# Kernel optimization log

Hardware: AMD Instinct MI355X
Metric: run time of the kernel (lower is better)

## Reference

```python
import jax, jax.numpy as jnp
import numpy as np

DIM = 256
HEADS = 4
DIM_HEAD = 32
HIDDEN = HEADS * DIM_HEAD  # 128
EPS = 1e-5


def setup_inputs() -> dict:
    key = jax.random.key(0)
    ks = jax.random.split(key, 6)
    B, H, W = 16, 64, 64
    x = jax.random.normal(ks[0], (B, DIM, H, W), dtype=jnp.float32)
    # 1x1 conv weights stored as [out_ch, in_ch]
    W_qkv = jax.random.normal(ks[1], (HIDDEN * 3, DIM), dtype=jnp.float32) * 0.02
    W_out = jax.random.normal(ks[2], (DIM, HIDDEN), dtype=jnp.float32) * 0.02
    b_out = jnp.zeros((DIM,), dtype=jnp.float32)
    gamma = jnp.ones((DIM,), dtype=jnp.float32)
    beta = jnp.zeros((DIM,), dtype=jnp.float32)
    return {"x": x, "W_qkv": W_qkv, "W_out": W_out, "b_out": b_out,
            "gamma": gamma, "beta": beta}


def reference(x, W_qkv, W_out, b_out, gamma, beta):
    b, c, h, w = x.shape
    n = h * w
    scale = DIM_HEAD ** -0.5
    # 1x1 conv == channel matmul
    qkv = jnp.einsum('bchw,oc->bohw', x, W_qkv)  # [b, 3*hidden, h, w]
    q, k, v = jnp.split(qkv, 3, axis=1)
    def to_heads(t):
        return t.reshape(b, HEADS, DIM_HEAD, n)  # b h d n
    q = jax.nn.softmax(to_heads(q), axis=-2) * scale  # softmax over d
    k = jax.nn.softmax(to_heads(k), axis=-1)           # softmax over n
    v = to_heads(v)
    # context: [b, h, d, e] — tiny 32x32 per head
    context = jnp.einsum('bhdn,bhen->bhde', k, v)
    out = jnp.einsum('bhde,bhdn->bhen', context, q)  # [b, h, e, n]
    out = out.reshape(b, HIDDEN, h, w)
    # output 1x1 conv with bias
    out = jnp.einsum('bchw,oc->bohw', out, W_out) + b_out[None, :, None, None]
    # GroupNorm(1, dim): normalize over (C,H,W) per sample, per-channel affine
    mean = out.mean(axis=(1, 2, 3), keepdims=True)
    var = out.var(axis=(1, 2, 3), keepdims=True)
    out = (out - mean) * jax.lax.rsqrt(var + EPS)
    return out * gamma[None, :, None, None] + beta[None, :, None, None]
```

## Files before the change

kernel.cpp:

```cpp
#include <hip/hip_runtime.h>

#define NN 4096
#define CIN 256
#define O3 384
#define HID 128
#define NHEAD 4
#define DH 32

typedef float f32x4 __attribute__((ext_vector_type(4)));
typedef _Float16 f16x8 __attribute__((ext_vector_type(8)));
typedef _Float16 f16x4 __attribute__((ext_vector_type(4)));
typedef _Float16 f16x2 __attribute__((ext_vector_type(2)));
typedef __fp16 fp16x2_raw __attribute__((ext_vector_type(2)));

__device__ __forceinline__ f16x2 pkrtz(float a, float b) {
  fp16x2_raw r = __builtin_amdgcn_cvt_pkrtz(a, b);
  return __builtin_bit_cast(f16x2, r);
}

__global__ __launch_bounds__(256) void prep(
    const float* __restrict__ Wqkv, const float* __restrict__ Wout,
    _Float16* __restrict__ WpkA, _Float16* __restrict__ WpkB,
    float* __restrict__ zbase, int nz) {
  const int bid = blockIdx.x, tid = threadIdx.x;
  if (bid < 48) {
    int t = bid * 256 + tid;
    int l = t & 63, mk = t >> 6;
    int k32 = mk & 7, m16 = mk >> 3;
    int row = m16 * 16 + (l & 15), k = k32 * 32 + (l >> 4) * 8;
    const float* s = Wqkv + (size_t)row * CIN + k;
    f16x8 o;
#pragma unroll
    for (int j = 0; j < 8; j++) o[j] = (_Float16)s[j];
    *(f16x8*)(WpkA + (size_t)t * 8) = o;
  } else if (bid < 64) {
    int t = (bid - 48) * 256 + tid;
    int l = t & 63, mk = t >> 6;
    int k32 = mk & 3, m16 = mk >> 2;
    int row = m16 * 16 + (l & 15), k = k32 * 32 + (l >> 4) * 8;
    const float* s = Wout + (size_t)row * HID + k;
    f16x8 o;
#pragma unroll
    for (int j = 0; j < 8; j++) o[j] = (_Float16)s[j];
    *(f16x8*)(WpkB + (size_t)t * 8) = o;
  } else {
    int i = (bid - 64) * 256 + tid;
    if (i < nz) zbase[i] = 0.f;
  }
}

__global__ __launch_bounds__(256) void gemm_qkv(
    const float* __restrict__ X, const _Float16* __restrict__ Wpk,
    _Float16* __restrict__ Yt) {
  __shared__ _Float16 Bs[128][40];
  const int mt = blockIdx.x;
  const int n0 = blockIdx.y * 128;
  const int b = blockIdx.z;
  const float* Xb = X + (size_t)b * CIN * NN;
  _Float16* Yb = Yt + (size_t)b * NN * O3;
  const int tid = threadIdx.x, l = tid & 63, wid = tid >> 6;
  const int wm = (wid >> 1) << 6, wn = (wid & 1) << 6;
  const int fr = l & 15, q = l >> 4, kq = q << 3;
  const int b_n = (tid & 31) << 2, b_kk = (tid >> 5) << 2;
  const int am16 = mt * 8 + (wm >> 4);

  f32x4 acc[4][4];
#pragma unroll
  for (int i = 0; i < 4; i++)
#pragma unroll
    for (int j = 0; j < 4; j++) acc[i][j] = (f32x4){0.f, 0.f, 0.f, 0.f};

  for (int k0 = 0; k0 < CIN; k0 += 32) {
    float xr[4][4];
#pragma unroll
    for (int i = 0; i < 4; i++)
      *(float4*)xr[i] = *(const float4*)(Xb + (size_t)(k0 + b_kk + i) * NN + n0 + b_n);
    f16x8 ah[4];
#pragma unroll
    for (int fm = 0; fm < 4; fm++)
      ah[fm] = *(const f16x8*)(Wpk + ((size_t)((am16 + fm) * 8 + (k0 >> 5)) * 64 + l) * 8);
    __syncthreads();
#pragma unroll
    for (int j = 0; j < 4; j++) {
      f16x2 p0 = pkrtz(xr[0][j], xr[1][j]);
      f16x2 p1 = pkrtz(xr[2][j], xr[3][j]);
      *(f16x4*)&Bs[b_n + j][b_kk] = (f16x4){p0[0], p0[1], p1[0], p1[1]};
    }
    __syncthreads();
    f16x8 bh[4];
#pragma unroll
    for (int fn = 0; fn < 4; fn++)
      bh[fn] = *(const f16x8*)&Bs[wn + fn * 16 + fr][kq];
#pragma unroll
    for (int fm = 0; fm < 4; fm++)
#pragma unroll
      for (int fn = 0; fn < 4; fn++)
        acc[fm][fn] = __builtin_amdgcn_mfma_f32_16x16x32_f16(ah[fm], bh[fn], acc[fm][fn], 0, 0, 0);
  }
#pragma unroll
  for (int fm = 0; fm < 4; fm++) {
    int mrow = mt * 128 + wm + fm * 16 + q * 4;
#pragma unroll
    for (int fn = 0; fn < 4; fn++) {
      int n = n0 + wn + fn * 16 + fr;
      f16x2 h0 = pkrtz(acc[fm][fn][0], acc[fm][fn][1]);
      f16x2 h1 = pkrtz(acc[fm][fn][2], acc[fm][fn][3]);
      *(f16x4*)(Yb + (size_t)n * O3 + mrow) = (f16x4){h0[0], h0[1], h1[0], h1[1]};
    }
  }
}

__global__ __launch_bounds__(256) void attn1(
    const _Float16* __restrict__ qkvt, float* __restrict__ ctx_raw,
    float* __restrict__ srow_raw) {
  const int h = blockIdx.x, b = blockIdx.y, ns = blockIdx.z;
  const _Float16* base = qkvt + (size_t)b * NN * O3;
  const _Float16* Kb = base + HID + h * DH;
  const _Float16* Vb = base + 2 * HID + h * DH;
  float* ctx = ctx_raw + (size_t)(b * NHEAD + h) * (DH * DH);
  float* srow = srow_raw + (size_t)(b * NHEAD + h) * DH;
  __shared__ __align__(16) float Es[64][36];
  __shared__ __align__(16) float Vs[64][36];
  __shared__ float ctxs[DH][DH + 1];
  __shared__ float srow_s[DH];
  const int tid = threadIdx.x, l = tid & 63, w = tid >> 6;
  const int d4 = (l >> 3) << 2, e4 = (l & 7) << 2;
  if (tid < DH) srow_s[tid] = 0.f;
  for (int i = tid; i < DH * (DH + 1); i += 256) (&ctxs[0][0])[i] = 0.f;
  float sacc[4] = {0.f, 0.f, 0.f, 0.f};
  float acc[4][4];
#pragma unroll
  for (int i = 0; i < 4; i++)
#pragma unroll
    for (int j = 0; j < 4; j++) acc[i][j] = 0.f;

  for (int c = 0; c < 8; c++) {
    const int n0 = ns * 512 + c * 64;
    const size_t roff = (size_t)(n0 + l) * O3 + w * 8;
    f16x8 kv = *(const f16x8*)(Kb + roff);
    f16x8 vv = *(const f16x8*)(Vb + roff);
    __syncthreads();
    float4 e0, e1, v0, v1;
    e0.x = __expf((float)kv[0]); e0.y = __expf((float)kv[1]);
    e0.z = __expf((float)kv[2]); e0.w = __expf((float)kv[3]);
    e1.x = __expf((float)kv[4]); e1.y = __expf((float)kv[5]);
    e1.z = __expf((float)kv[6]); e1.w = __expf((float)kv[7]);
    v0.x = (float)vv[0]; v0.y = (float)vv[1]; v0.z = (float)vv[2]; v0.w = (float)vv[3];
    v1.x = (float)vv[4]; v1.y = (float)vv[5]; v1.z = (float)vv[6]; v1.w = (float)vv[7];
    *(float4*)&Es[l][w * 8] = e0;
    *(float4*)&Es[l][w * 8 + 4] = e1;
    *(float4*)&Vs[l][w * 8] = v0;
    *(float4*)&Vs[l][w * 8 + 4] = v1;
    __syncthreads();
#pragma unroll
    for (int it = 0; it < 16; it++) {
      const int n = w + 4 * it;
      float ka[4], va[4];
      *(float4*)ka = *(const float4*)&Es[n][d4];
      *(float4*)va = *(const float4*)&Vs[n][e4];
#pragma unroll
      for (int i = 0; i < 4; i++) {
        sacc[i] += ka[i];
#pragma unroll
        for (int j = 0; j < 4; j++) acc[i][j] = fmaf(ka[i], va[j], acc[i][j]);
      }
    }
  }
  if ((l & 7) == 0) {
#pragma unroll
    for (int i = 0; i < 4; i++) atomicAdd(&srow_s[d4 + i], sacc[i]);
  }
#pragma unroll
  for (int i = 0; i < 4; i++)
#pragma unroll
    for (int j = 0; j < 4; j++) atomicAdd(&ctxs[d4 + i][e4 + j], acc[i][j]);
  __syncthreads();
  for (int i = tid; i < DH * DH; i += 256) atomicAdd(&ctx[i], ctxs[i >> 5][i & 31]);
  if (tid < DH) atomicAdd(&srow[tid], srow_s[tid]);
}

__global__ __launch_bounds__(256) void attn2(
    _Float16* __restrict__ qkvt, const float* __restrict__ ctx_raw,
    const float* __restrict__ srow_raw) {
  const int ns = blockIdx.x, h = blockIdx.y, b = blockIdx.z;
  const float* cg = ctx_raw + (size_t)(b * NHEAD + h) * (DH * DH);
  const float* sr = srow_raw + (size_t)(b * NHEAD + h) * DH;
  __shared__ float ctxs[DH][DH + 1];
  const int tid = threadIdx.x;
  for (int i = tid; i < DH * DH; i += 256) ctxs[i >> 5][i & 31] = cg[i] / sr[i >> 5];
  __syncthreads();
  const int n = ns * 256 + tid;
  _Float16* qp = qkvt + ((size_t)b * NN + n) * O3 + h * DH;
  float qv[DH];
#pragma unroll
  for (int i = 0; i < 4; i++) {
    f16x8 v = *(const f16x8*)(qp + i * 8);
#pragma unroll
    for (int j = 0; j < 8; j++) qv[i * 8 + j] = (float)v[j];
  }
  float m = -1e30f;
#pragma unroll
  for (int d = 0; d < DH; d++) m = fmaxf(m, qv[d]);
  float s = 0.f;
#pragma unroll
  for (int d = 0; d < DH; d++) { qv[d] = __expf(qv[d] - m); s += qv[d]; }
  float inv = 0.17677669529663687f / s;
#pragma unroll
  for (int d = 0; d < DH; d++) qv[d] *= inv;
#pragma unroll
  for (int eo = 0; eo < 4; eo++) {
    float o[8];
#pragma unroll
    for (int j = 0; j < 8; j++) o[j] = 0.f;
#pragma unroll
    for (int d = 0; d < DH; d++) {
      float qd = qv[d];
#pragma unroll
      for (int j = 0; j < 8; j++) o[j] = fmaf(ctxs[d][eo * 8 + j], qd, o[j]);
    }
    f16x2 h0 = pkrtz(o[0], o[1]);
    f16x2 h1 = pkrtz(o[2], o[3]);
    f16x2 h2 = pkrtz(o[4], o[5]);
    f16x2 h3 = pkrtz(o[6], o[7]);
    f16x8 ov = (f16x8){h0[0], h0[1], h1[0], h1[1], h2[0], h2[1], h3[0], h3[1]};
    *(f16x8*)(qp + eo * 8) = ov;
  }
}

__global__ __launch_bounds__(256) void gemm_proj(
    const _Float16* __restrict__ At, const _Float16* __restrict__ Wpk,
    const float* __restrict__ bias, float* __restrict__ out,
    double* __restrict__ stats) {
  __shared__ _Float16 Bs[128][40];
  const int mt = blockIdx.x;
  const int n0 = blockIdx.y * 128;
  const int b = blockIdx.z;
  const _Float16* Ab = At + (size_t)b * NN * O3;
  float* outb = out + (size_t)b * CIN * NN;
  const int tid = threadIdx.x, l = tid & 63, wid = tid >> 6;
  const int wm = (wid >> 1) << 6, wn = (wid & 1) << 6;
  const int fr = l & 15, q = l >> 4, kq = q << 3;
  const int am16 = mt * 8 + (wm >> 4);
  const int sr0 = tid >> 2, sc = (tid & 3) << 3;

  f32x4 acc[4][4];
#pragma unroll
  for (int i = 0; i < 4; i++)
#pragma unroll
    for (int j = 0; j < 4; j++) acc[i][j] = (f32x4){0.f, 0.f, 0.f, 0.f};

  for (int k0 = 0; k0 < HID; k0 += 32) {
    f16x8 v0 = *(const f16x8*)(Ab + (size_t)(n0 + sr0) * O3 + k0 + sc);
    f16x8 v1 = *(const f16x8*)(Ab + (size_t)(n0 + 64 + sr0) * O3 + k0 + sc);
    f16x8 ah[4];
#pragma unroll
    for (int fm = 0; fm < 4; fm++)
      ah[fm] = *(const f16x8*)(Wpk + ((size_t)((am16 + fm) * 4 + (k0 >> 5)) * 64 + l) * 8);
    __syncthreads();
    *(f16x8*)&Bs[sr0][sc] = v0;
    *(f16x8*)&Bs[64 + sr0][sc] = v1;
    __syncthreads();
    f16x8 bh[4];
#pragma unroll
    for (int fn = 0; fn < 4; fn++)
      bh[fn] = *(const f16x8*)&Bs[wn + fn * 16 + fr][kq];
#pragma unroll
    for (int fm = 0; fm < 4; fm++)
#pragma unroll
      for (int fn = 0; fn < 4; fn++)
        acc[fm][fn] = __builtin_amdgcn_mfma_f32_16x16x32_f16(ah[fm], bh[fn], acc[fm][fn], 0, 0, 0);
  }
  float lsum = 0.f, lsq = 0.f;
#pragma unroll
  for (int fm = 0; fm < 4; fm++) {
    int rowb = mt * 128 + wm + fm * 16 + q * 4;
#pragma unroll
    for (int r = 0; r < 4; r++) {
      float bv = bias[rowb + r];
      float* dst = outb + (size_t)(rowb + r) * NN + n0 + wn + fr;
#pragma unroll
      for (int fn = 0; fn < 4; fn++) {
        float v = acc[fm][fn][r] + bv;
        dst[fn * 16] = v;
        lsum += v;
        lsq += v * v;
      }
    }
  }
  double ds = (double)lsum, dq = (double)lsq;
#pragma unroll
  for (int off = 32; off; off >>= 1) {
    ds += __shfl_down(ds, off);
    dq += __shfl_down(dq, off);
  }
  __shared__ double sred[8];
  if (l == 0) { sred[wid] = ds; sred[4 + wid] = dq; }
  __syncthreads();
  if (tid == 0) {
    atomicAdd(&stats[b * 2 + 0], sred[0] + sred[1] + sred[2] + sred[3]);
    atomicAdd(&stats[b * 2 + 1], sred[4] + sred[5] + sred[6] + sred[7]);
  }
}

__global__ __launch_bounds__(256) void gn_norm(
    float* __restrict__ out, const double* __restrict__ stats,
    const float* __restrict__ gamma, const float* __restrict__ beta) {
  const int b = blockIdx.y;
  const double nels = (double)CIN * (double)NN;
  double S = stats[b * 2 + 0], Q2 = stats[b * 2 + 1];
  double mu = S / nels;
  double var = Q2 / nels - mu * mu;
  float mean = (float)mu;
  float rstd = (float)rsqrt(var + 1e-5);
  size_t i4 = (size_t)blockIdx.x * 256 + threadIdx.x;
  int c = (int)((i4 * 4) >> 12);
  float g = gamma[c] * rstd, bt = beta[c];
  float4* p = (float4*)(out + (size_t)b * CIN * NN) + i4;
  float4 v = *p;
  v.x = (v.x - mean) * g + bt;
  v.y = (v.y - mean) * g + bt;
  v.z = (v.z - mean) * g + bt;
  v.w = (v.w - mean) * g + bt;
  *p = v;
}

extern "C" void kernel_launch(void* const* d_in, const int* in_sizes, int n_in,
                              void* d_out, int out_size, void* d_ws, size_t ws_size,
                              hipStream_t stream) {
  const float* x     = (const float*)d_in[0];
  const float* Wqkv  = (const float*)d_in[1];
  const float* Wout  = (const float*)d_in[2];
  const float* bout  = (const float*)d_in[3];
  const float* gamma = (const float*)d_in[4];
  const float* beta  = (const float*)d_in[5];
  float* out = (float*)d_out;

  char* ws = (char*)d_ws;
  _Float16* qkvt = (_Float16*)ws;
  size_t off = (size_t)16 * NN * O3 * 2;
  _Float16* WpkA = (_Float16*)(ws + off); off += 48 * 256 * 8 * 2;
  _Float16* WpkB = (_Float16*)(ws + off); off += 16 * 256 * 8 * 2;
  float* ctxg = (float*)(ws + off); off += (size_t)16 * NHEAD * DH * DH * 4;
  float* srow = (float*)(ws + off); off += (size_t)16 * NHEAD * DH * 4;
  double* stats = (double*)(ws + off);

  const int nz = 16 * NHEAD * DH * DH + 16 * NHEAD * DH + 64;
  prep<<<64 + (nz + 255) / 256, 256, 0, stream>>>(Wqkv, Wout, WpkA, WpkB, ctxg, nz);
  gemm_qkv<<<dim3(3, 32, 16), 256, 0, stream>>>(x, WpkA, qkvt);
  attn1<<<dim3(NHEAD, 16, 8), 256, 0, stream>>>(qkvt, ctxg, srow);
  attn2<<<dim3(16, NHEAD, 16), 256, 0, stream>>>(qkvt, ctxg, srow);
  gemm_proj<<<dim3(2, 32, 16), 256, 0, stream>>>(qkvt, WpkB, bout, out, stats);
  gn_norm<<<dim3(1024, 16), 256, 0, stream>>>(out, stats, gamma, beta);
}
```

Measured before the change: 141.8 us.

## Stage full-K X tile in LDS once and loop over all QKV output tiles

The QKV projection kernel now loads a 64-column slab of X across all 256 input channels into shared memory once, converting it to fp16. Each block then loops over all three 128-row output tiles, so X is read from global memory once instead of three times. The per-k-step double sync is removed, at the cost of a larger shared-memory footprint, fewer columns per block and a smaller per-warp MFMA tile. It also raises the occupancy hint in launch bounds.

```diff
diff --git a/kernel.cpp b/kernel.cpp
--- a/kernel.cpp
+++ b/kernel.cpp
@@ -49,63 +49,77 @@
   }
 }
 
-__global__ __launch_bounds__(256) void gemm_qkv(
+__global__ __launch_bounds__(256, 4) void gemm_qkv(
     const float* __restrict__ X, const _Float16* __restrict__ Wpk,
     _Float16* __restrict__ Yt) {
-  __shared__ _Float16 Bs[128][40];
-  const int mt = blockIdx.x;
-  const int n0 = blockIdx.y * 128;
-  const int b = blockIdx.z;
+  __shared__ _Float16 Xs[8][64][40];
+  const int tid = threadIdx.x;
+  const int n0 = blockIdx.x * 64;
+  const int b = blockIdx.y;
   const float* Xb = X + (size_t)b * CIN * NN;
   _Float16* Yb = Yt + (size_t)b * NN * O3;
-  const int tid = threadIdx.x, l = tid & 63, wid = tid >> 6;
-  const int wm = (wid >> 1) << 6, wn = (wid & 1) << 6;
+
+  const int sc = tid & 15;
+  const int skq = (tid >> 4) * 4;
+  f32x4 xv[4][4];
+#pragma unroll
+  for (int ch = 0; ch < 4; ch++) {
+    const int kbase = ch * 64 + skq;
+#pragma unroll
+    for (int r = 0; r < 4; r++)
+      xv[ch][r] = *(const f32x4*)(Xb + (size_t)(kbase + r) * NN + n0 + sc * 4);
+  }
+#pragma unroll
+  for (int ch = 0; ch < 4; ch++) {
+    const int kb = ch * 2 + (skq >> 5);
+    const int kk = skq & 31;
+#pragma unroll
+    for (int j = 0; j < 4; j++) {
+      f16x2 p0 = pkrtz(xv[ch][0][j], xv[ch][1][j]);
+      f16x2 p1 = pkrtz(xv[ch][2][j], xv[ch][3][j]);
+      *(f16x4*)&Xs[kb][sc * 4 + j][kk] = (f16x4){p0[0], p0[1], p1[0], p1[1]};
+    }
+  }
+  __syncthreads();
+
+  const int l = tid & 63, w = tid >> 6;
+  const int wrow = (w >> 1) << 6;
+  const int wcol = (w & 1) << 5;
   const int fr = l & 15, q = l >> 4, kq = q << 3;
-  const int b_n = (tid & 31) << 2, b_kk = (tid >> 5) << 2;
-  const int am16 = mt * 8 + (wm >> 4);
-
-  f32x4 acc[4][4];
-#pragma unroll
-  for (int i = 0; i < 4; i++)
-#pragma unroll
-    for (int j = 0; j < 4; j++) acc[i][j] = (f32x4){0.f, 0.f, 0.f, 0.f};
-
-  for (int k0 = 0; k0 < CIN; k0 += 32) {
-    float xr[4][4];
+
+  for (int mtl = 0; mtl < 3; ++mtl) {
+    f32x4 acc[4][2];
 #pragma unroll
     for (int i = 0; i < 4; i++)
-      *(float4*)xr[i] = *(const float4*)(Xb + (size_t)(k0 + b_kk + i) * NN + n0 + b_n);
-    f16x8 ah[4];
-#pragma unroll
-    for (int fm = 0; fm < 4; fm++)
-      ah[fm] = *(const f16x8*)(Wpk + ((size_t)((am16 + fm) * 8 + (k0 >> 5)) * 64 + l) * 8);
-    __syncthreads();
-#pragma unroll
-    for (int j = 0; j < 4; j++) {
-      f16x2 p0 = pkrtz(xr[0][j], xr[1][j]);
-      f16x2 p1 = pkrtz(xr[2][j], xr[3][j]);
-      *(f16x4*)&Bs[b_n + j][b_kk] = (f16x4){p0[0], p0[1], p1[0], p1[1]};
-    }
-    __syncthreads();
-    f16x8 bh[4];
-#pragma unroll
-    for (int fn = 0; fn < 4; fn++)
-      bh[fn] = *(const f16x8*)&Bs[wn + fn * 16 + fr][kq];
-#pragma unroll
-    for (int fm = 0; fm < 4; fm++)
-#pragma unroll
-      for (int fn = 0; fn < 4; fn++)
-        acc[fm][fn] = __builtin_amdgcn_mfma_f32_16x16x32_f16(ah[fm], bh[fn], acc[fm][fn], 0, 0, 0);
-  }
-#pragma unroll
-  for (int fm = 0; fm < 4; fm++) {
-    int mrow = mt * 128 + wm + fm * 16 + q * 4;
-#pragma unroll
-    for (int fn = 0; fn < 4; fn++) {
-      int n = n0 + wn + fn * 16 + fr;
-      f16x2 h0 = pkrtz(acc[fm][fn][0], acc[fm][fn][1]);
-      f16x2 h1 = pkrtz(acc[fm][fn][2], acc[fm][fn][3]);
-      *(f16x4*)(Yb + (size_t)n * O3 + mrow) = (f16x4){h0[0], h0[1], h1[0], h1[1]};
+#pragma unroll
+      for (int j = 0; j < 2; j++) acc[i][j] = (f32x4){0.f, 0.f, 0.f, 0.f};
+    const int am16 = mtl * 8 + (wrow >> 4);
+#pragma unroll
+    for (int kb = 0; kb < 8; ++kb) {
+      f16x8 ah[4];
+#pragma unroll
+      for (int fm = 0; fm < 4; fm++)
+        ah[fm] = *(const f16x8*)(Wpk + ((size_t)((am16 + fm) * 8 + kb) * 64 + l) * 8);
+      f16x8 bh[2];
+#pragma unroll
+      for (int fn = 0; fn < 2; fn++)
+        bh[fn] = *(const f16x8*)&Xs[kb][wcol + fn * 16 + fr][kq];
+#pragma unroll
+      for (int fm = 0; fm < 4; fm++)
+#pragma unroll
+        for (int fn = 0; fn < 2; fn++)
+          acc[fm][fn] = __builtin_amdgcn_mfma_f32_16x16x32_f16(ah[fm], bh[fn], acc[fm][fn], 0, 0, 0);
+    }
+#pragma unroll
+    for (int fm = 0; fm < 4; fm++) {
+      int mrow = mtl * 128 + wrow + fm * 16 + q * 4;
+#pragma unroll
+      for (int fn = 0; fn < 2; fn++) {
+        int n = n0 + wcol + fn * 16 + fr;
+        f16x2 h0 = pkrtz(acc[fm][fn][0], acc[fm][fn][1]);
+        f16x2 h1 = pkrtz(acc[fm][fn][2], acc[fm][fn][3]);
+        *(f16x4*)(Yb + (size_t)n * O3 + mrow) = (f16x4){h0[0], h0[1], h1[0], h1[1]};
+      }
     }
   }
 }
@@ -346,7 +360,7 @@
 
   const int nz = 16 * NHEAD * DH * DH + 16 * NHEAD * DH + 64;
   prep<<<64 + (nz + 255) / 256, 256, 0, stream>>>(Wqkv, Wout, WpkA, WpkB, ctxg, nz);
-  gemm_qkv<<<dim3(3, 32, 16), 256, 0, stream>>>(x, WpkA, qkvt);
+  gemm_qkv<<<dim3(64, 16), 256, 0, stream>>>(x, WpkA, qkvt);
   attn1<<<dim3(NHEAD, 16, 8), 256, 0, stream>>>(qkvt, ctxg, srow);
   attn2<<<dim3(16, NHEAD, 16), 256, 0, stream>>>(qkvt, ctxg, srow);
   gemm_proj<<<dim3(2, 32, 16), 256, 0, stream>>>(qkvt, WpkB, bout, out, stats);
```

Result: slower. 167.5 us (+18.1%).

## Double-buffer QKV GEMM shared tiles with register prefetch and XCD-aware block swizzle

Applied to the files above, without the earlier changes.

The QKV projection GEMM now keeps two LDS buffers and prefetches the next X tile and weight fragments into registers while the MFMAs for the current tile run. This cuts the K-loop from two barriers per step to one. The grid is flattened to 1D, and block indices are remapped so consecutive blocks on the same XCD share the same X columns across the three M tiles, which should improve L2 reuse. The cost is more registers and LDS per block, which may lower occupancy.

```diff
diff --git a/kernel.cpp b/kernel.cpp
--- a/kernel.cpp
+++ b/kernel.cpp
@@ -52,10 +52,13 @@
 __global__ __launch_bounds__(256) void gemm_qkv(
     const float* __restrict__ X, const _Float16* __restrict__ Wpk,
     _Float16* __restrict__ Yt) {
-  __shared__ _Float16 Bs[128][40];
-  const int mt = blockIdx.x;
-  const int n0 = blockIdx.y * 128;
-  const int b = blockIdx.z;
+  __shared__ _Float16 Bs[2][128][40];
+  const int orig = blockIdx.x;
+  const int swz = (orig & 7) * 192 + (orig >> 3);
+  const int mt = swz % 3;
+  const int nb = swz / 3;
+  const int n0 = (nb & 31) << 7;
+  const int b  = nb >> 5;
   const float* Xb = X + (size_t)b * CIN * NN;
   _Float16* Yb = Yt + (size_t)b * NN * O3;
   const int tid = threadIdx.x, l = tid & 63, wid = tid >> 6;
@@ -64,39 +67,62 @@
   const int b_n = (tid & 31) << 2, b_kk = (tid >> 5) << 2;
   const int am16 = mt * 8 + (wm >> 4);
 
+#define LOADX(dst, t_) do { \
+    _Pragma("unroll") \
+    for (int r_ = 0; r_ < 4; r_++) \
+      dst[r_] = *(const f32x4*)(Xb + (size_t)((t_) * 32 + b_kk + r_) * NN + n0 + b_n); \
+  } while (0)
+#define LOADAH(dst, t_) do { \
+    _Pragma("unroll") \
+    for (int fm_ = 0; fm_ < 4; fm_++) \
+      dst[fm_] = *(const f16x8*)(Wpk + ((size_t)((am16 + fm_) * 8 + (t_)) * 64 + l) * 8); \
+  } while (0)
+#define CVTW(buf_, src) do { \
+    _Pragma("unroll") \
+    for (int j_ = 0; j_ < 4; j_++) { \
+      f16x2 p0_ = pkrtz(src[0][j_], src[1][j_]); \
+      f16x2 p1_ = pkrtz(src[2][j_], src[3][j_]); \
+      *(f16x4*)&Bs[buf_][b_n + j_][b_kk] = (f16x4){p0_[0], p0_[1], p1_[0], p1_[1]}; \
+    } } while (0)
+
+  f32x4 xr[2][4];
+  f16x8 ah[2][4];
   f32x4 acc[4][4];
 #pragma unroll
   for (int i = 0; i < 4; i++)
 #pragma unroll
     for (int j = 0; j < 4; j++) acc[i][j] = (f32x4){0.f, 0.f, 0.f, 0.f};
 
-  for (int k0 = 0; k0 < CIN; k0 += 32) {
-    float xr[4][4];
-#pragma unroll
-    for (int i = 0; i < 4; i++)
-      *(float4*)xr[i] = *(const float4*)(Xb + (size_t)(k0 + b_kk + i) * NN + n0 + b_n);
-    f16x8 ah[4];
+  LOADX(xr[0], 0);
+  CVTW(0, xr[0]);
+  LOADAH(ah[0], 0);
+  LOADX(xr[1], 1);
+  asm volatile("s_waitcnt lgkmcnt(0)" ::: "memory");
+  __builtin_amdgcn_s_barrier();
+  __builtin_amdgcn_sched_barrier(0);
+
+#pragma unroll
+  for (int t = 0; t < 8; t++) {
+    const int cur = t & 1, nxt = cur ^ 1;
+    f16x8 bh[4];
+#pragma unroll
+    for (int fn = 0; fn < 4; fn++)
+      bh[fn] = *(const f16x8*)&Bs[cur][wn + fn * 16 + fr][kq];
 #pragma unroll
     for (int fm = 0; fm < 4; fm++)
-      ah[fm] = *(const f16x8*)(Wpk + ((size_t)((am16 + fm) * 8 + (k0 >> 5)) * 64 + l) * 8);
-    __syncthreads();
-#pragma unroll
-    for (int j = 0; j < 4; j++) {
-      f16x2 p0 = pkrtz(xr[0][j], xr[1][j]);
-      f16x2 p1 = pkrtz(xr[2][j], xr[3][j]);
-      *(f16x4*)&Bs[b_n + j][b_kk] = (f16x4){p0[0], p0[1], p1[0], p1[1]};
-    }
-    __syncthreads();
-    f16x8 bh[4];
-#pragma unroll
-    for (int fn = 0; fn < 4; fn++)
-      bh[fn] = *(const f16x8*)&Bs[wn + fn * 16 + fr][kq];
-#pragma unroll
-    for (int fm = 0; fm < 4; fm++)
 #pragma unroll
       for (int fn = 0; fn < 4; fn++)
-        acc[fm][fn] = __builtin_amdgcn_mfma_f32_16x16x32_f16(ah[fm], bh[fn], acc[fm][fn], 0, 0, 0);
-  }
+        acc[fm][fn] = __builtin_amdgcn_mfma_f32_16x16x32_f16(ah[cur][fm], bh[fn], acc[fm][fn], 0, 0, 0);
+    if (t < 7) {
+      CVTW(nxt, xr[nxt]);
+      LOADAH(ah[nxt], t + 1);
+      if (t < 6) LOADX(xr[cur], t + 2);
+    }
+    asm volatile("s_waitcnt lgkmcnt(0)" ::: "memory");
+    __builtin_amdgcn_s_barrier();
+    __builtin_amdgcn_sched_barrier(0);
+  }
+
 #pragma unroll
   for (int fm = 0; fm < 4; fm++) {
     int mrow = mt * 128 + wm + fm * 16 + q * 4;
@@ -108,6 +134,9 @@
       *(f16x4*)(Yb + (size_t)n * O3 + mrow) = (f16x4){h0[0], h0[1], h1[0], h1[1]};
     }
   }
+#undef LOADX
+#undef LOADAH
+#undef CVTW
 }
 
 __global__ __launch_bounds__(256) void attn1(
@@ -346,7 +375,7 @@
 
   const int nz = 16 * NHEAD * DH * DH + 16 * NHEAD * DH + 64;
   prep<<<64 + (nz + 255) / 256, 256, 0, stream>>>(Wqkv, Wout, WpkA, WpkB, ctxg, nz);
-  gemm_qkv<<<dim3(3, 32, 16), 256, 0, stream>>>(x, WpkA, qkvt);
+  gemm_qkv<<<dim3(1536), 256, 0, stream>>>(x, WpkA, qkvt);
   attn1<<<dim3(NHEAD, 16, 8), 256, 0, stream>>>(qkvt, ctxg, srow);
   attn2<<<dim3(16, NHEAD, 16), 256, 0, stream>>>(qkvt, ctxg, srow);
   gemm_proj<<<dim3(2, 32, 16), 256, 0, stream>>>(qkvt, WpkB, bout, out, stats);
```

Result: faster. 133.0 us (-6.3%).

## Restructure QKV GEMM so each block covers all output rows and gathers X directly

Applied to the files above, without the earlier changes.

The QKV projection kernel now gives each block a 64-column strip with all 384 output rows, split as 96 rows per wave. This means X is read only once instead of three times across M tiles. The shared-memory staging and both barriers are removed: each lane gathers its B fragment straight from global memory with scalar strided loads and converts it in registers, and the k loop is fully unrolled. The cost is scalar, uncoalesced-per-lane loads of 16 consecutive floats across rows, plus higher register pressure from 24 accumulators. Launch bounds are set to 3 blocks per SM.

```diff
diff --git a/kernel.cpp b/kernel.cpp
--- a/kernel.cpp
+++ b/kernel.cpp
@@ -49,65 +49,71 @@
   }
 }
 
-__global__ __launch_bounds__(256) void gemm_qkv(
+__global__ __launch_bounds__(256, 3) void gemm_qkv(
     const float* __restrict__ X, const _Float16* __restrict__ Wpk,
     _Float16* __restrict__ Yt) {
-  __shared__ _Float16 Bs[128][40];
-  const int mt = blockIdx.x;
-  const int n0 = blockIdx.y * 128;
-  const int b = blockIdx.z;
+  const int n0 = blockIdx.x * 64;
+  const int b = blockIdx.y;
   const float* Xb = X + (size_t)b * CIN * NN;
   _Float16* Yb = Yt + (size_t)b * NN * O3;
-  const int tid = threadIdx.x, l = tid & 63, wid = tid >> 6;
-  const int wm = (wid >> 1) << 6, wn = (wid & 1) << 6;
+  const int tid = threadIdx.x, l = tid & 63, w = tid >> 6;
   const int fr = l & 15, q = l >> 4, kq = q << 3;
-  const int b_n = (tid & 31) << 2, b_kk = (tid >> 5) << 2;
-  const int am16 = mt * 8 + (wm >> 4);
-
-  f32x4 acc[4][4];
-#pragma unroll
-  for (int i = 0; i < 4; i++)
+  const int am16 = w * 6;
+  const float* xlane = Xb + (size_t)kq * NN + n0 + fr;
+
+#define GATHER(dst, t_, fn_) do { \
+    _Pragma("unroll") \
+    for (int j_ = 0; j_ < 8; j_++) \
+      dst[j_] = xlane[(size_t)((t_) * 32 + j_) * NN + (fn_) * 16]; \
+  } while (0)
+#define CVT(dst, s_) do { \
+    f16x2 a0_ = pkrtz(s_[0], s_[1]), a1_ = pkrtz(s_[2], s_[3]); \
+    f16x2 a2_ = pkrtz(s_[4], s_[5]), a3_ = pkrtz(s_[6], s_[7]); \
+    dst = (f16x8){a0_[0], a0_[1], a1_[0], a1_[1], a2_[0], a2_[1], a3_[0], a3_[1]}; \
+  } while (0)
+
+  f32x4 acc[6][4];
+#pragma unroll
+  for (int i = 0; i < 6; i++)
 #pragma unroll
     for (int j = 0; j < 4; j++) acc[i][j] = (f32x4){0.f, 0.f, 0.f, 0.f};
 
-  for (int k0 = 0; k0 < CIN; k0 += 32) {
-    float xr[4][4];
-#pragma unroll
-    for (int i = 0; i < 4; i++)
-      *(float4*)xr[i] = *(const float4*)(Xb + (size_t)(k0 + b_kk + i) * NN + n0 + b_n);
-    f16x8 ah[4];
-#pragma unroll
-    for (int fm = 0; fm < 4; fm++)
-      ah[fm] = *(const f16x8*)(Wpk + ((size_t)((am16 + fm) * 8 + (k0 >> 5)) * 64 + l) * 8);
-    __syncthreads();
-#pragma unroll
-    for (int j = 0; j < 4; j++) {
-      f16x2 p0 = pkrtz(xr[0][j], xr[1][j]);
-      f16x2 p1 = pkrtz(xr[2][j], xr[3][j]);
-      *(f16x4*)&Bs[b_n + j][b_kk] = (f16x4){p0[0], p0[1], p1[0], p1[1]};
-    }
-    __syncthreads();
+#pragma unroll
+  for (int t = 0; t < 8; t++) {
+    f16x8 ah[6];
+#pragma unroll
+    for (int fm = 0; fm < 6; fm++)
+      ah[fm] = *(const f16x8*)(Wpk + ((size_t)((am16 + fm) * 8 + t) * 64 + l) * 8);
+    float xa[8], xb[8];
     f16x8 bh[4];
+    GATHER(xa, t, 0);
+    GATHER(xb, t, 1);
+    CVT(bh[0], xa);
+    GATHER(xa, t, 2);
+    CVT(bh[1], xb);
+    GATHER(xb, t, 3);
+    CVT(bh[2], xa);
+    CVT(bh[3], xb);
 #pragma unroll
     for (int fn = 0; fn < 4; fn++)
-      bh[fn] = *(const f16x8*)&Bs[wn + fn * 16 + fr][kq];
-#pragma unroll
-    for (int fm = 0; fm < 4; fm++)
-#pragma unroll
-      for (int fn = 0; fn < 4; fn++)
+#pragma unroll
+      for (int fm = 0; fm < 6; fm++)
         acc[fm][fn] = __builtin_amdgcn_mfma_f32_16x16x32_f16(ah[fm], bh[fn], acc[fm][fn], 0, 0, 0);
   }
-#pragma unroll
-  for (int fm = 0; fm < 4; fm++) {
-    int mrow = mt * 128 + wm + fm * 16 + q * 4;
+
+#pragma unroll
+  for (int fm = 0; fm < 6; fm++) {
+    int mrow = (am16 + fm) * 16 + q * 4;
 #pragma unroll
     for (int fn = 0; fn < 4; fn++) {
-      int n = n0 + wn + fn * 16 + fr;
+      int n = n0 + fn * 16 + fr;
       f16x2 h0 = pkrtz(acc[fm][fn][0], acc[fm][fn][1]);
       f16x2 h1 = pkrtz(acc[fm][fn][2], acc[fm][fn][3]);
       *(f16x4*)(Yb + (size_t)n * O3 + mrow) = (f16x4){h0[0], h0[1], h1[0], h1[1]};
     }
   }
+#undef GATHER
+#undef CVT
 }
 
 __global__ __launch_bounds__(256) void attn1(
@@ -346,7 +352,7 @@
 
   const int nz = 16 * NHEAD * DH * DH + 16 * NHEAD * DH + 64;
   prep<<<64 + (nz + 255) / 256, 256, 0, stream>>>(Wqkv, Wout, WpkA, WpkB, ctxg, nz);
-  gemm_qkv<<<dim3(3, 32, 16), 256, 0, stream>>>(x, WpkA, qkvt);
+  gemm_qkv<<<dim3(64, 16), 256, 0, stream>>>(x, WpkA, qkvt);
   attn1<<<dim3(NHEAD, 16, 8), 256, 0, stream>>>(qkvt, ctxg, srow);
   attn2<<<dim3(16, NHEAD, 16), 256, 0, stream>>>(qkvt, ctxg, srow);
   gemm_proj<<<dim3(2, 32, 16), 256, 0, stream>>>(qkvt, WpkB, bout, out, stats);
```

Result: slower. 150.0 us (+5.8%).
